# Optimization experiments

Hardware: AMD Instinct MI355X
Metric: run time of the kernel (lower is better)

## Reference

```python
import jax, jax.numpy as jnp
import numpy as np

MODES = 256
WIDTH = 64
T_HIST = 1
T_FUT = 1
BATCH = 64
S = 8192


def setup_inputs() -> dict:
    key = jax.random.key(0)
    ks = jax.random.split(key, 12)
    scale = 1.0 / (WIDTH * WIDTH)
    inp = {
        "u": jax.random.normal(ks[0], (BATCH, S, T_HIST), dtype=jnp.float32),
        # lifting layer: Linear(T_HIST+1 -> WIDTH), stored [in, out]
        "fc0_w": jax.random.normal(ks[1], (T_HIST + 1, WIDTH), dtype=jnp.float32) * 0.5,
        "fc0_b": jax.random.normal(ks[2], (WIDTH,), dtype=jnp.float32) * 0.1,
        # 4 spectral conv layers, complex weights stored as real/imag parts
        "sw_r": scale * jax.random.uniform(ks[3], (4, WIDTH, WIDTH, MODES), dtype=jnp.float32),
        "sw_i": scale * jax.random.uniform(ks[4], (4, WIDTH, WIDTH, MODES), dtype=jnp.float32),
        # 4 pointwise (1x1 conv) layers: weight [out,in], bias [out]
        "pw_w": jax.random.normal(ks[5], (4, WIDTH, WIDTH), dtype=jnp.float32) * (1.0 / np.sqrt(WIDTH)),
        "pw_b": jax.random.normal(ks[6], (4, WIDTH), dtype=jnp.float32) * 0.1,
        # projection head
        "fc1_w": jax.random.normal(ks[7], (WIDTH, 128), dtype=jnp.float32) * (1.0 / np.sqrt(WIDTH)),
        "fc1_b": jax.random.normal(ks[8], (128,), dtype=jnp.float32) * 0.1,
        "fc2_w": jax.random.normal(ks[9], (128, T_FUT), dtype=jnp.float32) * (1.0 / np.sqrt(128)),
        "fc2_b": jax.random.normal(ks[10], (T_FUT,), dtype=jnp.float32) * 0.1,
    }
    return inp


def _spectral_conv(x, wr, wi):
    # x: [b, c_in, s] real; weights: [c_in, c_out, MODES] (real/imag parts)
    s = x.shape[-1]
    xf = jnp.fft.rfft(x)                     # [b, c_in, s//2+1] complex
    w = wr + 1j * wi
    om = jnp.einsum('bix,iox->box', xf[:, :, :MODES], w)  # [b, c_out, MODES]
    out_ft = jnp.zeros((x.shape[0], wr.shape[1], s // 2 + 1), dtype=om.dtype)
    out_ft = out_ft.at[:, :, :MODES].set(om)
    return jnp.fft.irfft(out_ft, n=s)        # [b, c_out, s] real


def reference(u, fc0_w, fc0_b, sw_r, sw_i, pw_w, pw_b, fc1_w, fc1_b, fc2_w, fc2_b):
    b, s, _ = u.shape
    grid = jnp.broadcast_to(jnp.linspace(0.0, 1.0, s, dtype=u.dtype)[None, :, None], (b, s, 1))
    x = jnp.concatenate([u, grid], axis=-1)              # [b, s, 2]
    x = x @ fc0_w + fc0_b                                # [b, s, W]
    x = jnp.transpose(x, (0, 2, 1))                      # [b, W, s]
    for l in range(4):
        x1 = _spectral_conv(x, sw_r[l], sw_i[l])
        x2 = jnp.einsum('oi,bis->bos', pw_w[l], x) + pw_b[l][None, :, None]
        x = x1 + x2
        if l < 3:
            x = jax.nn.gelu(x, approximate=False)
    x = jnp.transpose(x, (0, 2, 1))                      # [b, s, W]
    x = jax.nn.gelu(x @ fc1_w + fc1_b, approximate=False)
    x = x @ fc2_w + fc2_b                                # [b, s, T_FUT]
    return x
```

## Files before the change

kernel.cpp:

```cpp
#include <hip/hip_runtime.h>
#include <hip/hip_bf16.h>
#include <math.h>

#define BB 64
#define CC 64
#define SS 8192
#define HS 4096
#define NMODE 256
#define KK2 512

typedef __attribute__((ext_vector_type(8))) short short8;
typedef __attribute__((ext_vector_type(16))) float f32x16;

#define VMW8 asm volatile("s_waitcnt vmcnt(8)" ::: "memory")
#define VMW0 asm volatile("s_waitcnt vmcnt(0)" ::: "memory")
#define SBAR asm volatile("s_barrier" ::: "memory")

__device__ __forceinline__ float gelu_exact(float v) {
    return 0.5f * v * (1.0f + erff(v * 0.7071067811865476f));
}
__device__ __forceinline__ float b2f(ushort u) {
    return __uint_as_float(((unsigned int)u) << 16);
}
__device__ __forceinline__ ushort f2b(float v) {
    __hip_bfloat16 h = __float2bfloat16(v);
    return *(ushort*)&h;
}
__device__ __forceinline__ void split2(float v, ushort& h, ushort& l) {
    h = f2b(v);
    l = f2b(v - b2f(h));
}
__device__ __forceinline__ int colk(int c) {
    return (c < 256) ? (c & ~1) : (((c - 256) & ~1) | 1);
}
__device__ __forceinline__ void dma16(const ushort* g, ushort* l) {
    __builtin_amdgcn_global_load_lds((const __attribute__((address_space(1))) void*)g,
                                     (__attribute__((address_space(3))) void*)l, 16, 0, 0);
}

__global__ void build_T1p(ushort* __restrict__ h, ushort* __restrict__ l) {
    int c = blockIdx.x;
    int n = blockIdx.y * 256 + threadIdx.x;
    int k = colk(c), ri = c & 1;
    int m = (n * k) & (SS - 1);
    float th = (float)m * (6.283185307179586476925f / (float)SS);
    float s, co;
    sincosf(th, &s, &co);
    float v = ri ? -s : co;
    ushort hh, ll;
    split2(v, hh, ll);
    h[(size_t)c * HS + n] = hh;
    l[(size_t)c * HS + n] = ll;
}

__global__ void build_T2r(ushort* __restrict__ h, ushort* __restrict__ l) {
    int n = blockIdx.x;
    int c = blockIdx.y * 256 + threadIdx.x;
    int k = colk(c), ri = c & 1;
    int m = (n * k) & (SS - 1);
    float th = (float)m * (6.283185307179586476925f / (float)SS);
    float s, co;
    sincosf(th, &s, &co);
    float v = ri ? -s : co;
    ushort hh, ll;
    split2(v, hh, ll);
    h[(size_t)n * KK2 + c] = hh;
    l[(size_t)n * KK2 + c] = ll;
}

__global__ void zero_xf(float* __restrict__ p) {
    size_t i = ((size_t)blockIdx.x * 256 + threadIdx.x) * 4;
    *(float4*)&p[i] = make_float4(0.f, 0.f, 0.f, 0.f);
}

__global__ void lift_kernel(const float* __restrict__ u, const float* __restrict__ w0,
                            const float* __restrict__ b0, ushort* __restrict__ Eh,
                            ushort* __restrict__ El, ushort* __restrict__ Oh,
                            ushort* __restrict__ Ol) {
    int n = blockIdx.x * 256 + threadIdx.x;
    int c = blockIdx.y;
    int b = blockIdx.z;
    float g1 = (float)n * (1.0f / (float)(SS - 1));
    float g2 = (float)(n + HS) * (1.0f / (float)(SS - 1));
    float v1 = u[b * SS + n] * w0[c] + g1 * w0[CC + c] + b0[c];
    float v2 = u[b * SS + n + HS] * w0[c] + g2 * w0[CC + c] + b0[c];
    float E = v1 + v2, O = v1 - v2;
    ushort hh, ll;
    size_t idx = (size_t)(b * CC + c) * HS + n;
    split2(E, hh, ll);
    Eh[idx] = hh;
    El[idx] = ll;
    split2(O, hh, ll);
    Oh[idx] = hh;
    Ol[idx] = ll;
}

__global__ __launch_bounds__(256, 2) void dft_mfma(
    const ushort* __restrict__ Eh, const ushort* __restrict__ El,
    const ushort* __restrict__ Oh, const ushort* __restrict__ Ol,
    const ushort* __restrict__ t1h, const ushort* __restrict__ t1l,
    float* __restrict__ Xf) {
    __shared__ __align__(16) ushort SM[32768];
    const int t = threadIdx.x;
    const int L = blockIdx.x;
    const int gq = L >> 5, j = L & 31;
    const int c0 = (j >> 3) * 128;
    const int m0 = ((gq & 3) * 8 + (j & 7)) * 128;
    const int kz = (gq >> 2) * 1024;
    const ushort* __restrict__ Ahp = (c0 < 256) ? Eh : Oh;
    const ushort* __restrict__ Alp = (c0 < 256) ? El : Ol;
    const int lane = t & 63, w = t >> 6;
    const int wm = (w >> 1) * 64, wn = (w & 1) * 64;
    const int l32 = lane & 31, lh = lane >> 5;

    f32x16 acc[2][2];
#pragma unroll
    for (int i = 0; i < 2; i++)
#pragma unroll
        for (int jj = 0; jj < 2; jj++) acc[i][jj] = (f32x16)0.f;

    const size_t aoff = (size_t)(m0 + lane) * HS + w * 8;
    const size_t boff = (size_t)(c0 + lane) * HS + w * 8;
    const size_t r64 = (size_t)64 * HS;

    auto stage = [&](int kt, int bsel) {
        ushort* base = SM + bsel * 16384;
        ushort* dAh = base + w * 1024;
        ushort* dAl = base + 4096 + w * 1024;
        ushort* dBh = base + 8192 + w * 1024;
        ushort* dBl = base + 12288 + w * 1024;
        dma16(Ahp + aoff + kt, dAh);
        dma16(Ahp + aoff + r64 + kt, dAh + 512);
        dma16(Alp + aoff + kt, dAl);
        dma16(Alp + aoff + r64 + kt, dAl + 512);
        dma16(t1h + boff + kt, dBh);
        dma16(t1h + boff + r64 + kt, dBh + 512);
        dma16(t1l + boff + kt, dBl);
        dma16(t1l + boff + r64 + kt, dBl + 512);
    };
    auto compute = [&](int bsel) {
        const ushort* As_h = SM + bsel * 16384;
        const ushort* As_l = As_h + 4096;
        const ushort* Bs_h = As_h + 8192;
        const ushort* Bs_l = As_h + 12288;
#pragma unroll
        for (int s2 = 0; s2 < 2; s2++) {
            const int kg = s2 * 2 + lh;
            short8 ah[2], al[2], bh2[2], bl2[2];
#pragma unroll
            for (int mt = 0; mt < 2; mt++) {
                int off = (kg * 128 + wm + mt * 32 + l32) * 8;
                ah[mt] = *(const short8*)&As_h[off];
                al[mt] = *(const short8*)&As_l[off];
            }
#pragma unroll
            for (int nt = 0; nt < 2; nt++) {
                int off = (kg * 128 + wn + nt * 32 + l32) * 8;
                bh2[nt] = *(const short8*)&Bs_h[off];
                bl2[nt] = *(const short8*)&Bs_l[off];
            }
#pragma unroll
            for (int nt = 0; nt < 2; nt++)
#pragma unroll
                for (int mt = 0; mt < 2; mt++) {
                    acc[mt][nt] = __builtin_amdgcn_mfma_f32_32x32x16_bf16(ah[mt], bh2[nt], acc[mt][nt], 0, 0, 0);
                    acc[mt][nt] = __builtin_amdgcn_mfma_f32_32x32x16_bf16(ah[mt], bl2[nt], acc[mt][nt], 0, 0, 0);
                    acc[mt][nt] = __builtin_amdgcn_mfma_f32_32x32x16_bf16(al[mt], bh2[nt], acc[mt][nt], 0, 0, 0);
                }
        }
    };

    stage(kz, 0);
#pragma unroll 1
    for (int st = 0; st < 32; st++) {
        const int buf = st & 1;
        if (st < 31) {
            stage(kz + (st + 1) * 32, buf ^ 1);
            VMW8;
        } else {
            VMW0;
        }
        SBAR;
        compute(buf);
        SBAR;
    }
#pragma unroll
    for (int mt = 0; mt < 2; mt++)
#pragma unroll
        for (int nt = 0; nt < 2; nt++) {
            int col = c0 + wn + nt * 32 + l32;
#pragma unroll
            for (int reg = 0; reg < 16; reg++) {
                int row = m0 + wm + mt * 32 + (reg & 3) + 8 * (reg >> 2) + 4 * lh;
                atomicAdd(&Xf[(size_t)row * KK2 + col], acc[mt][nt][reg]);
            }
        }
}

__global__ __launch_bounds__(256) void mode_mix(const float* __restrict__ Xf,
                                                const float* __restrict__ swr,
                                                const float* __restrict__ swi,
                                                ushort* __restrict__ omh,
                                                ushort* __restrict__ oml, int l) {
    int k = threadIdx.x;
    int bg = blockIdx.x * 2;
    int og = blockIdx.y * 2;
    const int cp = ((k & 1) << 8) | ((k >> 1) << 1);
    float ar[2][2] = {}, ai[2][2] = {};
#pragma unroll 2
    for (int i = 0; i < CC; i++) {
        float2 x0 = *(const float2*)&Xf[((size_t)(bg + 0) * CC + i) * KK2 + cp];
        float2 x1 = *(const float2*)&Xf[((size_t)(bg + 1) * CC + i) * KK2 + cp];
        size_t wb = ((size_t)(l * CC + i) * CC + og) * NMODE + k;
        float wr0 = swr[wb], wi0 = swi[wb];
        float wr1 = swr[wb + NMODE], wi1 = swi[wb + NMODE];
        ar[0][0] += x0.x * wr0 - x0.y * wi0;
        ai[0][0] += x0.x * wi0 + x0.y * wr0;
        ar[0][1] += x0.x * wr1 - x0.y * wi1;
        ai[0][1] += x0.x * wi1 + x0.y * wr1;
        ar[1][0] += x1.x * wr0 - x1.y * wi0;
        ai[1][0] += x1.x * wi0 + x1.y * wr0;
        ar[1][1] += x1.x * wr1 - x1.y * wi1;
        ai[1][1] += x1.x * wi1 + x1.y * wr1;
    }
    float ck = (k == 0) ? (1.0f / (float)SS) : (2.0f / (float)SS);
#pragma unroll
    for (int b2 = 0; b2 < 2; b2++)
#pragma unroll
        for (int oo = 0; oo < 2; oo++) {
            float re = ar[b2][oo] * ck;
            float im = ai[b2][oo] * ck;
            ushort hr, lr2, hi2, li2;
            split2(re, hr, lr2);
            split2(im, hi2, li2);
            size_t base = ((size_t)(bg + b2) * CC + og + oo) * KK2 + cp;
            *(ushort2*)&omh[base] = make_ushort2(hr, hi2);
            *(ushort2*)&oml[base] = make_ushort2(lr2, li2);
        }
}

__global__ __launch_bounds__(256, 2) void inv_mfma(
    const ushort* __restrict__ omh, const ushort* __restrict__ oml,
    const ushort* __restrict__ t2h, const ushort* __restrict__ t2l,
    const float* __restrict__ pww, const float* __restrict__ pwb,
    ushort* __restrict__ Eh, ushort* __restrict__ El,
    ushort* __restrict__ Oh, ushort* __restrict__ Ol, int l, int gel) {
    __shared__ __align__(16) ushort SM[32768];
    const int t = threadIdx.x;
    const int n0 = blockIdx.x * 128;
    const int row0 = blockIdx.y * 128;
    const int lane = t & 63, w = t >> 6;
    const int wm = (w >> 1) * 64, wn = (w & 1) * 64;
    const int l32 = lane & 31, lh = lane >> 5;

    f32x16 aP[2][2], aQ[2][2];
#pragma unroll
    for (int i = 0; i < 2; i++)
#pragma unroll
        for (int jj = 0; jj < 2; jj++) {
            aP[i][jj] = (f32x16)0.f;
            aQ[i][jj] = (f32x16)0.f;
        }

    const size_t aoff = (size_t)(row0 + lane) * KK2 + w * 8;
    const size_t boff = (size_t)(n0 + lane) * KK2 + w * 8;
    const size_t rstep = (size_t)64 * KK2;

    auto stage1 = [&](int st, int bsel) {
        const int kt = st * 32;
        ushort* base = SM + bsel * 16384;
        ushort* dAh = base + w * 1024;
        ushort* dAl = base + 4096 + w * 1024;
        ushort* dBh = base + 8192 + w * 1024;
        ushort* dBl = base + 12288 + w * 1024;
        dma16(omh + aoff + kt, dAh);
        dma16(omh + aoff + rstep + kt, dAh + 512);
        dma16(oml + aoff + kt, dAl);
        dma16(oml + aoff + rstep + kt, dAl + 512);
        dma16(t2h + boff + kt, dBh);
        dma16(t2h + boff + rstep + kt, dBh + 512);
        dma16(t2l + boff + kt, dBl);
        dma16(t2l + boff + rstep + kt, dBl + 512);
    };
    const size_t xsrc = (size_t)(row0 + (w >> 1) * 64 + (w & 1) * 32 + (lane >> 4)) * HS +
                        n0 + (lane & 15) * 8;
    auto stage2 = [&](const ushort* src, int bsel) {
        ushort* dX = SM + bsel * 16384 + w * 4096;
#pragma unroll
        for (int q = 0; q < 8; q++) dma16(src + xsrc + (size_t)q * 4 * HS, dX + q * 512);
    };
    auto compute1 = [&](f32x16 (&acc)[2][2], const int bsel) {
        const ushort* base = SM + bsel * 16384;
#pragma unroll
        for (int s2 = 0; s2 < 2; s2++) {
            const int kg = s2 * 2 + lh;
            short8 ah[2], al[2], bh2[2], bl2[2];
#pragma unroll
            for (int mt = 0; mt < 2; mt++) {
                int off = (kg * 128 + wm + mt * 32 + l32) * 8;
                ah[mt] = *(const short8*)&base[off];
                al[mt] = *(const short8*)&base[4096 + off];
            }
#pragma unroll
            for (int nt = 0; nt < 2; nt++) {
                int off = (kg * 128 + wn + nt * 32 + l32) * 8;
                bh2[nt] = *(const short8*)&base[8192 + off];
                bl2[nt] = *(const short8*)&base[12288 + off];
            }
#pragma unroll
            for (int nt = 0; nt < 2; nt++)
#pragma unroll
                for (int mt = 0; mt < 2; mt++) {
                    acc[mt][nt] = __builtin_amdgcn_mfma_f32_32x32x16_bf16(ah[mt], bh2[nt], acc[mt][nt], 0, 0, 0);
                    acc[mt][nt] = __builtin_amdgcn_mfma_f32_32x32x16_bf16(ah[mt], bl2[nt], acc[mt][nt], 0, 0, 0);
                    acc[mt][nt] = __builtin_amdgcn_mfma_f32_32x32x16_bf16(al[mt], bh2[nt], acc[mt][nt], 0, 0, 0);
                }
        }
    };

    stage1(0, 0);
#pragma unroll 1
    for (int st = 0; st < 8; st++) {
        const int buf = st & 1;
        stage1(st + 1, buf ^ 1);
        VMW8;
        SBAR;
        compute1(aP, buf);
        SBAR;
    }
#pragma unroll 1
    for (int st = 8; st < 15; st++) {
        const int buf = st & 1;
        stage1(st + 1, buf ^ 1);
        VMW8;
        SBAR;
        compute1(aQ, buf);
        SBAR;
    }
    {
        stage2(Eh, 0);
        VMW8;
        SBAR;
        compute1(aQ, 1);
        SBAR;
    }
#pragma unroll
    for (int mt = 0; mt < 2; mt++)
#pragma unroll
        for (int nt = 0; nt < 2; nt++) {
            f32x16 p = aP[mt][nt];
            aP[mt][nt] = p + aQ[mt][nt];
            aQ[mt][nt] = p - aQ[mt][nt];
        }
    short8 pah[4][2], pal[4][2];
#pragma unroll
    for (int ks = 0; ks < 4; ks++)
#pragma unroll
        for (int mt = 0; mt < 2; mt++) {
            const float* pp = &pww[(size_t)(l * CC + mt * 32 + l32) * CC + ks * 16 + lh * 8];
            float4 pa = *(const float4*)pp;
            float4 pb = *(const float4*)(pp + 4);
            float pv[8] = {pa.x, pa.y, pa.z, pa.w, pb.x, pb.y, pb.z, pb.w};
#pragma unroll
            for (int e = 0; e < 8; e++) {
                ushort h2, l2;
                split2(0.5f * pv[e], h2, l2);
                pah[ks][mt][e] = (short)h2;
                pal[ks][mt][e] = (short)l2;
            }
        }
    const int bsw = w >> 1;
    const ushort* const srcs[4] = {Eh, El, Oh, Ol};
#pragma unroll
    for (int r = 0; r < 4; r++) {
        const int buf = r & 1;
        const bool isO = (r >= 2), isHi = !(r & 1);
        if (r < 3) {
            stage2(srcs[r + 1], buf ^ 1);
            VMW8;
        } else {
            VMW0;
        }
        SBAR;
        const ushort* base = SM + buf * 16384;
#pragma unroll
        for (int ks = 0; ks < 4; ks++) {
            short8 bf[2], nbf[2];
#pragma unroll
            for (int nt = 0; nt < 2; nt++) {
                const int rb = (bsw * 64 + ks * 16 + lh * 8) * 128 + wn + nt * 32 + l32;
#pragma unroll
                for (int jj = 0; jj < 8; jj++) bf[nt][jj] = (short)base[rb + jj * 128];
                if (isO) {
#pragma unroll
                    for (int jj = 0; jj < 8; jj++)
                        nbf[nt][jj] = (short)(bf[nt][jj] ^ (short)0x8000);
                }
            }
#pragma unroll
            for (int nt = 0; nt < 2; nt++)
#pragma unroll
                for (int mt = 0; mt < 2; mt++) {
                    aP[mt][nt] = __builtin_amdgcn_mfma_f32_32x32x16_bf16(pah[ks][mt], bf[nt], aP[mt][nt], 0, 0, 0);
                    aQ[mt][nt] = __builtin_amdgcn_mfma_f32_32x32x16_bf16(pah[ks][mt], isO ? nbf[nt] : bf[nt], aQ[mt][nt], 0, 0, 0);
                    if (isHi) {
                        aP[mt][nt] = __builtin_amdgcn_mfma_f32_32x32x16_bf16(pal[ks][mt], bf[nt], aP[mt][nt], 0, 0, 0);
                        aQ[mt][nt] = __builtin_amdgcn_mfma_f32_32x32x16_bf16(pal[ks][mt], isO ? nbf[nt] : bf[nt], aQ[mt][nt], 0, 0, 0);
                    }
                }
        }
        if (r < 3) SBAR;
    }
#pragma unroll
    for (int mt = 0; mt < 2; mt++)
#pragma unroll
        for (int nt = 0; nt < 2; nt++)
#pragma unroll
            for (int reg = 0; reg < 16; reg++) {
                int roffs = (reg & 3) + 8 * (reg >> 2) + 4 * lh;
                float bias = pwb[l * CC + mt * 32 + roffs];
                float uu = aP[mt][nt][reg] + bias;
                float vv = aQ[mt][nt][reg] + bias;
                if (gel) {
                    uu = gelu_exact(uu);
                    vv = gelu_exact(vv);
                }
                float EE = uu + vv, OO = uu - vv;
                ushort h2, l2;
                size_t gg = (size_t)(row0 + wm + mt * 32 + roffs) * HS + n0 + wn + nt * 32 + l32;
                split2(EE, h2, l2);
                Eh[gg] = h2;
                El[gg] = l2;
                split2(OO, h2, l2);
                Oh[gg] = h2;
                Ol[gg] = l2;
            }
}

__global__ __launch_bounds__(256, 3) void head_kernel(
    const ushort* __restrict__ Eh, const ushort* __restrict__ El,
    const ushort* __restrict__ Oh, const ushort* __restrict__ Ol,
    const float* __restrict__ w1, const float* __restrict__ b1,
    const float* __restrict__ w2, const float* __restrict__ b2,
    float* __restrict__ out) {
    __shared__ __align__(16) ushort Xh[4096];
    __shared__ __align__(16) ushort Xl[4096];
    __shared__ __align__(16) ushort Wh[8192];
    __shared__ __align__(16) ushort Wl[8192];
    __shared__ float part[4][64];
    const int b = blockIdx.y;
    const int n0 = blockIdx.x * 64;
    const int t = threadIdx.x;
    const int lane = t & 63, w = t >> 6;
    const int l32 = lane & 31, lh = lane >> 5;
    const float sg = (n0 < HS) ? 0.5f : -0.5f;
    const int nc = n0 & (HS - 1);
    {
        const int n = lane;
        const size_t gx = (size_t)(b * CC + w * 16) * HS + nc + n;
        short8 fh[2], fl[2];
#pragma unroll
        for (int cc = 0; cc < 16; cc++) {
            size_t g = gx + (size_t)cc * HS;
            float e = b2f(Eh[g]) + b2f(El[g]);
            float o = b2f(Oh[g]) + b2f(Ol[g]);
            float x = 0.5f * e + sg * o;
            ushort hh, ll;
            split2(x, hh, ll);
            fh[cc >> 3][cc & 7] = (short)hh;
            fl[cc >> 3][cc & 7] = (short)ll;
        }
        const int kg0 = w * 2;
#pragma unroll
        for (int q = 0; q < 2; q++) {
            *(short8*)&Xh[((kg0 + q) * 64 + n) * 8] = fh[q];
            *(short8*)&Xl[((kg0 + q) * 64 + n) * 8] = fl[q];
        }
    }
    {
        const int j = t & 127, half = t >> 7;
#pragma unroll
        for (int q = 0; q < 4; q++) {
            const int kg = half * 4 + q;
            short8 fh, fl;
#pragma unroll
            for (int e = 0; e < 8; e++) {
                int c = kg * 8 + e;
                ushort hh, ll;
                split2(w1[c * 128 + j], hh, ll);
                fh[e] = (short)hh;
                fl[e] = (short)ll;
            }
            *(short8*)&Wh[(kg * 128 + j) * 8] = fh;
            *(short8*)&Wl[(kg * 128 + j) * 8] = fl;
        }
    }
    __syncthreads();
    f32x16 acc[2];
    acc[0] = (f32x16)0.f;
    acc[1] = (f32x16)0.f;
#pragma unroll
    for (int ks = 0; ks < 4; ks++) {
        const int kg = ks * 2 + lh;
        const int offa = (kg * 128 + w * 32 + l32) * 8;
        short8 awh = *(const short8*)&Wh[offa];
        short8 awl = *(const short8*)&Wl[offa];
#pragma unroll
        for (int nt = 0; nt < 2; nt++) {
            const int offb = (kg * 64 + nt * 32 + l32) * 8;
            short8 bxh = *(const short8*)&Xh[offb];
            short8 bxl = *(const short8*)&Xl[offb];
            acc[nt] = __builtin_amdgcn_mfma_f32_32x32x16_bf16(awh, bxh, acc[nt], 0, 0, 0);
            acc[nt] = __builtin_amdgcn_mfma_f32_32x32x16_bf16(awh, bxl, acc[nt], 0, 0, 0);
            acc[nt] = __builtin_amdgcn_mfma_f32_32x32x16_bf16(awl, bxh, acc[nt], 0, 0, 0);
        }
    }
#pragma unroll
    for (int nt = 0; nt < 2; nt++) {
        float s = 0.f;
#pragma unroll
        for (int reg = 0; reg < 16; reg++) {
            const int j0 = w * 32 + (reg & 3) + 8 * (reg >> 2) + 4 * lh;
            s += gelu_exact(acc[nt][reg] + b1[j0]) * w2[j0];
        }
        s += __shfl_xor(s, 32);
        part[w][nt * 32 + l32] = s;
    }
    __syncthreads();
    if (t < 64)
        out[b * SS + n0 + t] = part[0][t] + part[1][t] + part[2][t] + part[3][t] + b2[0];
}

extern "C" void kernel_launch(void* const* d_in, const int* in_sizes, int n_in,
                              void* d_out, int out_size, void* d_ws, size_t ws_size,
                              hipStream_t stream) {
    (void)in_sizes; (void)n_in; (void)out_size; (void)ws_size;
    const float* u = (const float*)d_in[0];
    const float* fc0_w = (const float*)d_in[1];
    const float* fc0_b = (const float*)d_in[2];
    const float* sw_r = (const float*)d_in[3];
    const float* sw_i = (const float*)d_in[4];
    const float* pw_w = (const float*)d_in[5];
    const float* pw_b = (const float*)d_in[6];
    const float* fc1_w = (const float*)d_in[7];
    const float* fc1_b = (const float*)d_in[8];
    const float* fc2_w = (const float*)d_in[9];
    const float* fc2_b = (const float*)d_in[10];
    float* out = (float*)d_out;

    char* ws = (char*)d_ws;
    ushort* Eh = (ushort*)ws;
    ushort* El = (ushort*)(ws + 33554432);
    ushort* Oh = (ushort*)(ws + 67108864);
    ushort* Ol = (ushort*)(ws + 100663296);
    ushort* t1h = (ushort*)(ws + 134217728);
    ushort* t1l = (ushort*)(ws + 138412032);
    ushort* t2h = (ushort*)(ws + 142606336);
    ushort* t2l = (ushort*)(ws + 146800640);
    ushort* omh = (ushort*)(ws + 150994944);
    ushort* oml = (ushort*)(ws + 155189248);
    float* Xf = (float*)(ws + 159383552);

    build_T1p<<<dim3(KK2, HS / 256), 256, 0, stream>>>(t1h, t1l);
    build_T2r<<<dim3(HS, KK2 / 256), 256, 0, stream>>>(t2h, t2l);
    lift_kernel<<<dim3(HS / 256, CC, BB), 256, 0, stream>>>(u, fc0_w, fc0_b, Eh, El,
                                                            Oh, Ol);
    for (int l = 0; l < 4; l++) {
        zero_xf<<<dim3(2048), 256, 0, stream>>>(Xf);
        dft_mfma<<<dim3(512), 256, 0, stream>>>(Eh, El, Oh, Ol, t1h, t1l, Xf);
        mode_mix<<<dim3(BB / 2, CC / 2), 256, 0, stream>>>(Xf, sw_r, sw_i, omh, oml, l);
        inv_mfma<<<dim3(HS / 128, 32), 256, 0, stream>>>(
            omh, oml, t2h, t2l, pw_w, pw_b, Eh, El, Oh, Ol, l, (l < 3) ? 1 : 0);
    }
    head_kernel<<<dim3(SS / 64, BB), 256, 0, stream>>>(Eh, El, Oh, Ol, fc1_w, fc1_b,
                                                       fc2_w, fc2_b, out);
}
```

Baseline: 1.315 ms.

## Halve DFT K-chunk and inverse N-tile to raise occupancy and grid size

The forward DFT GEMM now splits K into twice as many chunks (1024 blocks, 16-wide K steps), halving its LDS footprint so three blocks fit per CU, and each wave stages a single source array. The inverse GEMM tile shrinks from 128 to 64 columns, doubling its grid, with LDS cut to 24K shorts and a reworked per-wave staging split. Both kernels move to launch bounds of 3 to allow more resident waves to hide latency. The trade-offs are more atomic adds into Xf from the extra K splits, smaller per-block reuse, and more barrier iterations per unit of work.

```diff
diff --git a/kernel.cpp b/kernel.cpp
--- a/kernel.cpp
+++ b/kernel.cpp
@@ -12,7 +12,8 @@
 typedef __attribute__((ext_vector_type(8))) short short8;
 typedef __attribute__((ext_vector_type(16))) float f32x16;
 
-#define VMW8 asm volatile("s_waitcnt vmcnt(8)" ::: "memory")
+#define VMW6 asm volatile("s_waitcnt vmcnt(6)" ::: "memory")
+#define VMW4 asm volatile("s_waitcnt vmcnt(4)" ::: "memory")
 #define VMW0 asm volatile("s_waitcnt vmcnt(0)" ::: "memory")
 #define SBAR asm volatile("s_barrier" ::: "memory")
 
@@ -95,18 +96,18 @@
     Ol[idx] = ll;
 }
 
-__global__ __launch_bounds__(256, 2) void dft_mfma(
+__global__ __launch_bounds__(256, 3) void dft_mfma(
     const ushort* __restrict__ Eh, const ushort* __restrict__ El,
     const ushort* __restrict__ Oh, const ushort* __restrict__ Ol,
     const ushort* __restrict__ t1h, const ushort* __restrict__ t1l,
     float* __restrict__ Xf) {
-    __shared__ __align__(16) ushort SM[32768];
+    __shared__ __align__(16) ushort SM[16384];
     const int t = threadIdx.x;
     const int L = blockIdx.x;
     const int gq = L >> 5, j = L & 31;
     const int c0 = (j >> 3) * 128;
     const int m0 = ((gq & 3) * 8 + (j & 7)) * 128;
-    const int kz = (gq >> 2) * 1024;
+    const int kz = (gq >> 2) * 512;
     const ushort* __restrict__ Ahp = (c0 < 256) ? Eh : Oh;
     const ushort* __restrict__ Alp = (c0 < 256) ? El : Ol;
     const int lane = t & 63, w = t >> 6;
@@ -119,55 +120,42 @@
 #pragma unroll
         for (int jj = 0; jj < 2; jj++) acc[i][jj] = (f32x16)0.f;
 
-    const size_t aoff = (size_t)(m0 + lane) * HS + w * 8;
-    const size_t boff = (size_t)(c0 + lane) * HS + w * 8;
+    const ushort* const srcw = (w == 0) ? Ahp : (w == 1) ? Alp : (w == 2) ? t1h : t1l;
+    const int rbase = (w < 2) ? m0 : c0;
+    const size_t soff = (size_t)(rbase + lane) * HS;
     const size_t r64 = (size_t)64 * HS;
 
     auto stage = [&](int kt, int bsel) {
-        ushort* base = SM + bsel * 16384;
-        ushort* dAh = base + w * 1024;
-        ushort* dAl = base + 4096 + w * 1024;
-        ushort* dBh = base + 8192 + w * 1024;
-        ushort* dBl = base + 12288 + w * 1024;
-        dma16(Ahp + aoff + kt, dAh);
-        dma16(Ahp + aoff + r64 + kt, dAh + 512);
-        dma16(Alp + aoff + kt, dAl);
-        dma16(Alp + aoff + r64 + kt, dAl + 512);
-        dma16(t1h + boff + kt, dBh);
-        dma16(t1h + boff + r64 + kt, dBh + 512);
-        dma16(t1l + boff + kt, dBl);
-        dma16(t1l + boff + r64 + kt, dBl + 512);
+        ushort* dst = SM + bsel * 8192 + w * 2048;
+        dma16(srcw + soff + kt, dst);
+        dma16(srcw + soff + r64 + kt, dst + 512);
+        dma16(srcw + soff + kt + 8, dst + 1024);
+        dma16(srcw + soff + r64 + kt + 8, dst + 1536);
     };
     auto compute = [&](int bsel) {
-        const ushort* As_h = SM + bsel * 16384;
-        const ushort* As_l = As_h + 4096;
-        const ushort* Bs_h = As_h + 8192;
-        const ushort* Bs_l = As_h + 12288;
-#pragma unroll
-        for (int s2 = 0; s2 < 2; s2++) {
-            const int kg = s2 * 2 + lh;
-            short8 ah[2], al[2], bh2[2], bl2[2];
+        const ushort* base = SM + bsel * 8192;
+        const int kg = lh;
+        short8 ah[2], al[2], bh2[2], bl2[2];
+#pragma unroll
+        for (int mt = 0; mt < 2; mt++) {
+            int off = (kg * 128 + wm + mt * 32 + l32) * 8;
+            ah[mt] = *(const short8*)&base[off];
+            al[mt] = *(const short8*)&base[2048 + off];
+        }
+#pragma unroll
+        for (int nt = 0; nt < 2; nt++) {
+            int off = (kg * 128 + wn + nt * 32 + l32) * 8;
+            bh2[nt] = *(const short8*)&base[4096 + off];
+            bl2[nt] = *(const short8*)&base[6144 + off];
+        }
+#pragma unroll
+        for (int nt = 0; nt < 2; nt++)
 #pragma unroll
             for (int mt = 0; mt < 2; mt++) {
-                int off = (kg * 128 + wm + mt * 32 + l32) * 8;
-                ah[mt] = *(const short8*)&As_h[off];
-                al[mt] = *(const short8*)&As_l[off];
-            }
-#pragma unroll
-            for (int nt = 0; nt < 2; nt++) {
-                int off = (kg * 128 + wn + nt * 32 + l32) * 8;
-                bh2[nt] = *(const short8*)&Bs_h[off];
-                bl2[nt] = *(const short8*)&Bs_l[off];
-            }
-#pragma unroll
-            for (int nt = 0; nt < 2; nt++)
-#pragma unroll
-                for (int mt = 0; mt < 2; mt++) {
-                    acc[mt][nt] = __builtin_amdgcn_mfma_f32_32x32x16_bf16(ah[mt], bh2[nt], acc[mt][nt], 0, 0, 0);
-                    acc[mt][nt] = __builtin_amdgcn_mfma_f32_32x32x16_bf16(ah[mt], bl2[nt], acc[mt][nt], 0, 0, 0);
-                    acc[mt][nt] = __builtin_amdgcn_mfma_f32_32x32x16_bf16(al[mt], bh2[nt], acc[mt][nt], 0, 0, 0);
-                }
-        }
+                acc[mt][nt] = __builtin_amdgcn_mfma_f32_32x32x16_bf16(ah[mt], bh2[nt], acc[mt][nt], 0, 0, 0);
+                acc[mt][nt] = __builtin_amdgcn_mfma_f32_32x32x16_bf16(ah[mt], bl2[nt], acc[mt][nt], 0, 0, 0);
+                acc[mt][nt] = __builtin_amdgcn_mfma_f32_32x32x16_bf16(al[mt], bh2[nt], acc[mt][nt], 0, 0, 0);
+            }
     };
 
     stage(kz, 0);
@@ -175,8 +163,8 @@
     for (int st = 0; st < 32; st++) {
         const int buf = st & 1;
         if (st < 31) {
-            stage(kz + (st + 1) * 32, buf ^ 1);
-            VMW8;
+            stage(kz + (st + 1) * 16, buf ^ 1);
+            VMW4;
         } else {
             VMW0;
         }
@@ -239,82 +227,72 @@
         }
 }
 
-__global__ __launch_bounds__(256, 2) void inv_mfma(
+__global__ __launch_bounds__(256, 3) void inv_mfma(
     const ushort* __restrict__ omh, const ushort* __restrict__ oml,
     const ushort* __restrict__ t2h, const ushort* __restrict__ t2l,
     const float* __restrict__ pww, const float* __restrict__ pwb,
     ushort* __restrict__ Eh, ushort* __restrict__ El,
     ushort* __restrict__ Oh, ushort* __restrict__ Ol, int l, int gel) {
-    __shared__ __align__(16) ushort SM[32768];
+    __shared__ __align__(16) ushort SM[24576];
     const int t = threadIdx.x;
-    const int n0 = blockIdx.x * 128;
+    const int n0 = blockIdx.x * 64;
     const int row0 = blockIdx.y * 128;
     const int lane = t & 63, w = t >> 6;
-    const int wm = (w >> 1) * 64, wn = (w & 1) * 64;
+    const int wm = (w >> 1) * 64, wn = (w & 1) * 32;
     const int l32 = lane & 31, lh = lane >> 5;
 
-    f32x16 aP[2][2], aQ[2][2];
-#pragma unroll
-    for (int i = 0; i < 2; i++)
-#pragma unroll
-        for (int jj = 0; jj < 2; jj++) {
-            aP[i][jj] = (f32x16)0.f;
-            aQ[i][jj] = (f32x16)0.f;
-        }
-
-    const size_t aoff = (size_t)(row0 + lane) * KK2 + w * 8;
-    const size_t boff = (size_t)(n0 + lane) * KK2 + w * 8;
-    const size_t rstep = (size_t)64 * KK2;
+    f32x16 aP[2], aQ[2];
+    aP[0] = (f32x16)0.f;
+    aP[1] = (f32x16)0.f;
+    aQ[0] = (f32x16)0.f;
+    aQ[1] = (f32x16)0.f;
+
+    const int sel = w >> 1, p = w & 1;
+    const ushort* const Asrc = sel ? oml : omh;
+    const ushort* const Bsrc = sel ? t2l : t2h;
+    const size_t aoff = (size_t)(row0 + lane) * KK2;
+    const size_t boff = (size_t)(n0 + lane) * KK2;
+    const size_t r64 = (size_t)64 * KK2;
 
     auto stage1 = [&](int st, int bsel) {
-        const int kt = st * 32;
-        ushort* base = SM + bsel * 16384;
-        ushort* dAh = base + w * 1024;
-        ushort* dAl = base + 4096 + w * 1024;
-        ushort* dBh = base + 8192 + w * 1024;
-        ushort* dBl = base + 12288 + w * 1024;
-        dma16(omh + aoff + kt, dAh);
-        dma16(omh + aoff + rstep + kt, dAh + 512);
-        dma16(oml + aoff + kt, dAl);
-        dma16(oml + aoff + rstep + kt, dAl + 512);
-        dma16(t2h + boff + kt, dBh);
-        dma16(t2h + boff + rstep + kt, dBh + 512);
-        dma16(t2l + boff + kt, dBl);
-        dma16(t2l + boff + rstep + kt, dBl + 512);
+        const int kt = st * 32 + 2 * p * 8;
+        ushort* dA = SM + bsel * 12288 + sel * 4096 + 2 * p * 1024;
+        ushort* dB = SM + bsel * 12288 + 8192 + sel * 2048 + 2 * p * 512;
+        dma16(Asrc + aoff + kt, dA);
+        dma16(Asrc + aoff + r64 + kt, dA + 512);
+        dma16(Asrc + aoff + kt + 8, dA + 1024);
+        dma16(Asrc + aoff + r64 + kt + 8, dA + 1536);
+        dma16(Bsrc + boff + kt, dB);
+        dma16(Bsrc + boff + kt + 8, dB + 512);
     };
-    const size_t xsrc = (size_t)(row0 + (w >> 1) * 64 + (w & 1) * 32 + (lane >> 4)) * HS +
-                        n0 + (lane & 15) * 8;
+    const size_t xsrc = (size_t)(row0 + (w >> 1) * 64 + (w & 1) * 32 + (lane >> 3)) * HS +
+                        n0 + (lane & 7) * 8;
     auto stage2 = [&](const ushort* src, int bsel) {
-        ushort* dX = SM + bsel * 16384 + w * 4096;
-#pragma unroll
-        for (int q = 0; q < 8; q++) dma16(src + xsrc + (size_t)q * 4 * HS, dX + q * 512);
+        ushort* dX = SM + bsel * 12288 + (w >> 1) * 4096 + (w & 1) * 2048;
+#pragma unroll
+        for (int q = 0; q < 4; q++) dma16(src + xsrc + (size_t)q * 8 * HS, dX + q * 512);
     };
-    auto compute1 = [&](f32x16 (&acc)[2][2], const int bsel) {
-        const ushort* base = SM + bsel * 16384;
+    auto compute1 = [&](f32x16* acc, const int bsel) {
+        const ushort* base = SM + bsel * 12288;
 #pragma unroll
         for (int s2 = 0; s2 < 2; s2++) {
             const int kg = s2 * 2 + lh;
-            short8 ah[2], al[2], bh2[2], bl2[2];
+            short8 ah[2], al[2];
 #pragma unroll
             for (int mt = 0; mt < 2; mt++) {
                 int off = (kg * 128 + wm + mt * 32 + l32) * 8;
                 ah[mt] = *(const short8*)&base[off];
                 al[mt] = *(const short8*)&base[4096 + off];
             }
-#pragma unroll
-            for (int nt = 0; nt < 2; nt++) {
-                int off = (kg * 128 + wn + nt * 32 + l32) * 8;
-                bh2[nt] = *(const short8*)&base[8192 + off];
-                bl2[nt] = *(const short8*)&base[12288 + off];
-            }
-#pragma unroll
-            for (int nt = 0; nt < 2; nt++)
-#pragma unroll
-                for (int mt = 0; mt < 2; mt++) {
-                    acc[mt][nt] = __builtin_amdgcn_mfma_f32_32x32x16_bf16(ah[mt], bh2[nt], acc[mt][nt], 0, 0, 0);
-                    acc[mt][nt] = __builtin_amdgcn_mfma_f32_32x32x16_bf16(ah[mt], bl2[nt], acc[mt][nt], 0, 0, 0);
-                    acc[mt][nt] = __builtin_amdgcn_mfma_f32_32x32x16_bf16(al[mt], bh2[nt], acc[mt][nt], 0, 0, 0);
-                }
+            const int offb = (kg * 64 + wn + l32) * 8;
+            short8 bh = *(const short8*)&base[8192 + offb];
+            short8 bl = *(const short8*)&base[10240 + offb];
+#pragma unroll
+            for (int mt = 0; mt < 2; mt++) {
+                acc[mt] = __builtin_amdgcn_mfma_f32_32x32x16_bf16(ah[mt], bh, acc[mt], 0, 0, 0);
+                acc[mt] = __builtin_amdgcn_mfma_f32_32x32x16_bf16(ah[mt], bl, acc[mt], 0, 0, 0);
+                acc[mt] = __builtin_amdgcn_mfma_f32_32x32x16_bf16(al[mt], bh, acc[mt], 0, 0, 0);
+            }
         }
     };
 
@@ -323,7 +301,7 @@
     for (int st = 0; st < 8; st++) {
         const int buf = st & 1;
         stage1(st + 1, buf ^ 1);
-        VMW8;
+        VMW6;
         SBAR;
         compute1(aP, buf);
         SBAR;
@@ -332,26 +310,24 @@
     for (int st = 8; st < 15; st++) {
         const int buf = st & 1;
         stage1(st + 1, buf ^ 1);
-        VMW8;
+        VMW6;
         SBAR;
         compute1(aQ, buf);
         SBAR;
     }
     {
         stage2(Eh, 0);
-        VMW8;
+        VMW4;
         SBAR;
         compute1(aQ, 1);
         SBAR;
     }
 #pragma unroll
-    for (int mt = 0; mt < 2; mt++)
-#pragma unroll
-        for (int nt = 0; nt < 2; nt++) {
-            f32x16 p = aP[mt][nt];
-            aP[mt][nt] = p + aQ[mt][nt];
-            aQ[mt][nt] = p - aQ[mt][nt];
-        }
+    for (int mt = 0; mt < 2; mt++) {
+        f32x16 pp2 = aP[mt];
+        aP[mt] = pp2 + aQ[mt];
+        aQ[mt] = pp2 - aQ[mt];
+    }
     short8 pah[4][2], pal[4][2];
 #pragma unroll
     for (int ks = 0; ks < 4; ks++)
@@ -377,64 +353,56 @@
         const bool isO = (r >= 2), isHi = !(r & 1);
         if (r < 3) {
             stage2(srcs[r + 1], buf ^ 1);
-            VMW8;
+            VMW4;
         } else {
             VMW0;
         }
         SBAR;
-        const ushort* base = SM + buf * 16384;
+        const ushort* base = SM + buf * 12288;
 #pragma unroll
         for (int ks = 0; ks < 4; ks++) {
-            short8 bf[2], nbf[2];
-#pragma unroll
-            for (int nt = 0; nt < 2; nt++) {
-                const int rb = (bsw * 64 + ks * 16 + lh * 8) * 128 + wn + nt * 32 + l32;
-#pragma unroll
-                for (int jj = 0; jj < 8; jj++) bf[nt][jj] = (short)base[rb + jj * 128];
-                if (isO) {
-#pragma unroll
-                    for (int jj = 0; jj < 8; jj++)
-                        nbf[nt][jj] = (short)(bf[nt][jj] ^ (short)0x8000);
+            short8 bf, nbf;
+            const int rb = (bsw * 64 + ks * 16 + lh * 8) * 64 + wn + l32;
+#pragma unroll
+            for (int jj = 0; jj < 8; jj++) bf[jj] = (short)base[rb + jj * 64];
+            if (isO) {
+#pragma unroll
+                for (int jj = 0; jj < 8; jj++) nbf[jj] = (short)(bf[jj] ^ (short)0x8000);
+            }
+#pragma unroll
+            for (int mt = 0; mt < 2; mt++) {
+                aP[mt] = __builtin_amdgcn_mfma_f32_32x32x16_bf16(pah[ks][mt], bf, aP[mt], 0, 0, 0);
+                aQ[mt] = __builtin_amdgcn_mfma_f32_32x32x16_bf16(pah[ks][mt], isO ? nbf : bf, aQ[mt], 0, 0, 0);
+                if (isHi) {
+                    aP[mt] = __builtin_amdgcn_mfma_f32_32x32x16_bf16(pal[ks][mt], bf, aP[mt], 0, 0, 0);
+                    aQ[mt] = __builtin_amdgcn_mfma_f32_32x32x16_bf16(pal[ks][mt], isO ? nbf : bf, aQ[mt], 0, 0, 0);
                 }
             }
-#pragma unroll
-            for (int nt = 0; nt < 2; nt++)
-#pragma unroll
-                for (int mt = 0; mt < 2; mt++) {
-                    aP[mt][nt] = __builtin_amdgcn_mfma_f32_32x32x16_bf16(pah[ks][mt], bf[nt], aP[mt][nt], 0, 0, 0);
-                    aQ[mt][nt] = __builtin_amdgcn_mfma_f32_32x32x16_bf16(pah[ks][mt], isO ? nbf[nt] : bf[nt], aQ[mt][nt], 0, 0, 0);
-                    if (isHi) {
-                        aP[mt][nt] = __builtin_amdgcn_mfma_f32_32x32x16_bf16(pal[ks][mt], bf[nt], aP[mt][nt], 0, 0, 0);
-                        aQ[mt][nt] = __builtin_amdgcn_mfma_f32_32x32x16_bf16(pal[ks][mt], isO ? nbf[nt] : bf[nt], aQ[mt][nt], 0, 0, 0);
-                    }
-                }
         }
         if (r < 3) SBAR;
     }
 #pragma unroll
     for (int mt = 0; mt < 2; mt++)
 #pragma unroll
-        for (int nt = 0; nt < 2; nt++)
-#pragma unroll
-            for (int reg = 0; reg < 16; reg++) {
-                int roffs = (reg & 3) + 8 * (reg >> 2) + 4 * lh;
-                float bias = pwb[l * CC + mt * 32 + roffs];
-                float uu = aP[mt][nt][reg] + bias;
-                float vv = aQ[mt][nt][reg] + bias;
-                if (gel) {
-                    uu = gelu_exact(uu);
-                    vv = gelu_exact(vv);
-                }
-                float EE = uu + vv, OO = uu - vv;
-                ushort h2, l2;
-                size_t gg = (size_t)(row0 + wm + mt * 32 + roffs) * HS + n0 + wn + nt * 32 + l32;
-                split2(EE, h2, l2);
-                Eh[gg] = h2;
-                El[gg] = l2;
-                split2(OO, h2, l2);
-                Oh[gg] = h2;
-                Ol[gg] = l2;
-            }
+        for (int reg = 0; reg < 16; reg++) {
+            int roffs = (reg & 3) + 8 * (reg >> 2) + 4 * lh;
+            float bias = pwb[l * CC + mt * 32 + roffs];
+            float uu = aP[mt][reg] + bias;
+            float vv = aQ[mt][reg] + bias;
+            if (gel) {
+                uu = gelu_exact(uu);
+                vv = gelu_exact(vv);
+            }
+            float EE = uu + vv, OO = uu - vv;
+            ushort h2, l2;
+            size_t gg = (size_t)(row0 + wm + mt * 32 + roffs) * HS + n0 + wn + l32;
+            split2(EE, h2, l2);
+            Eh[gg] = h2;
+            El[gg] = l2;
+            split2(OO, h2, l2);
+            Oh[gg] = h2;
+            Ol[gg] = l2;
+        }
 }
 
 __global__ __launch_bounds__(256, 3) void head_kernel(
@@ -567,9 +535,9 @@
                                                             Oh, Ol);
     for (int l = 0; l < 4; l++) {
         zero_xf<<<dim3(2048), 256, 0, stream>>>(Xf);
-        dft_mfma<<<dim3(512), 256, 0, stream>>>(Eh, El, Oh, Ol, t1h, t1l, Xf);
+        dft_mfma<<<dim3(1024), 256, 0, stream>>>(Eh, El, Oh, Ol, t1h, t1l, Xf);
         mode_mix<<<dim3(BB / 2, CC / 2), 256, 0, stream>>>(Xf, sw_r, sw_i, omh, oml, l);
-        inv_mfma<<<dim3(HS / 128, 32), 256, 0, stream>>>(
+        inv_mfma<<<dim3(HS / 64, 32), 256, 0, stream>>>(
             omh, oml, t2h, t2l, pw_w, pw_b, Eh, El, Oh, Ol, l, (l < 3) ? 1 : 0);
     }
     head_kernel<<<dim3(SS / 64, BB), 256, 0, stream>>>(Eh, El, Oh, Ol, fc1_w, fc1_b,
```

Result: slower. 1.688 ms (+28.4%).
